# Performance work log

Hardware: AMD Instinct MI355X
Metric: run time of the kernel (lower is better)

The kernel has to match this reference:

```python
import jax, jax.numpy as jnp
import numpy as np

PARA_CH = 256
FEATURE_CH = 256
PI = 3.14159  # matches the literal in the torch source


def _linear_params(key, fan_in, fan_out):
    kw, kb = jax.random.split(key)
    bound = 1.0 / np.sqrt(fan_in)
    W = jax.random.uniform(kw, (fan_in, fan_out), minval=-bound, maxval=bound, dtype=jnp.float32)
    b = jax.random.uniform(kb, (fan_out,), minval=-bound, maxval=bound, dtype=jnp.float32)
    return W, b


def setup_inputs() -> dict:
    key = jax.random.key(0)
    ks = jax.random.split(key, 6)
    feature_map = jax.random.normal(ks[0], (4, FEATURE_CH, 128, 128), dtype=jnp.float32)
    para_code = jax.random.normal(ks[1], (4, PARA_CH), dtype=jnp.float32)
    W1, b1 = _linear_params(ks[2], PARA_CH, PARA_CH)
    Ws, bs = _linear_params(ks[3], PARA_CH, FEATURE_CH)
    Wr, br = _linear_params(ks[4], PARA_CH, FEATURE_CH)
    Wt, bt = _linear_params(ks[5], PARA_CH, 2 * FEATURE_CH)
    return {"feature_map": feature_map, "para_code": para_code,
            "W1": W1, "b1": b1, "Ws": Ws, "bs": bs,
            "Wr": Wr, "br": br, "Wt": Wt, "bt": bt}


def _coord_1d(n):
    # align_corners=True-style normalized coordinates, as in make_coordinate_grid_3d
    return 2.0 * (jnp.arange(n, dtype=jnp.float32) / (n - 1)) - 1.0


def _trilinear_sample_zeros(vol, gx, gy, gz):
    """F.grid_sample 5D equivalent: mode='bilinear' (trilinear), padding_mode='zeros',
    align_corners=False. vol: [B,D,H,W] (channel dim of size 1 squeezed out);
    gx,gy,gz: [B,Do,Ho,Wo] normalized coords. Returns [B,Do,Ho,Wo]."""
    B, D, H, W = vol.shape
    ix = ((gx + 1.0) * W - 1.0) * 0.5
    iy = ((gy + 1.0) * H - 1.0) * 0.5
    iz = ((gz + 1.0) * D - 1.0) * 0.5
    x0f, y0f, z0f = jnp.floor(ix), jnp.floor(iy), jnp.floor(iz)
    wx, wy, wz = ix - x0f, iy - y0f, iz - z0f
    x0 = x0f.astype(jnp.int32); x1 = x0 + 1
    y0 = y0f.astype(jnp.int32); y1 = y0 + 1
    z0 = z0f.astype(jnp.int32); z1 = z0 + 1
    vflat = vol.reshape(B, -1)

    def gather(zi, yi, xi):
        valid = (zi >= 0) & (zi < D) & (yi >= 0) & (yi < H) & (xi >= 0) & (xi < W)
        zc = jnp.clip(zi, 0, D - 1)
        yc = jnp.clip(yi, 0, H - 1)
        xc = jnp.clip(xi, 0, W - 1)
        flat = (zc * H + yc) * W + xc  # [B,Do,Ho,Wo]
        v = jnp.take_along_axis(vflat, flat.reshape(B, -1), axis=1).reshape(flat.shape)
        return jnp.where(valid, v, 0.0)

    out = (gather(z0, y0, x0) * (1 - wz) * (1 - wy) * (1 - wx)
           + gather(z0, y0, x1) * (1 - wz) * (1 - wy) * wx
           + gather(z0, y1, x0) * (1 - wz) * wy * (1 - wx)
           + gather(z0, y1, x1) * (1 - wz) * wy * wx
           + gather(z1, y0, x0) * wz * (1 - wy) * (1 - wx)
           + gather(z1, y0, x1) * wz * (1 - wy) * wx
           + gather(z1, y1, x0) * wz * wy * (1 - wx)
           + gather(z1, y1, x1) * wz * wy * wx)
    return out


def reference(feature_map, para_code, W1, b1, Ws, bs, Wr, br, Wt, bt):
    B, C, H, W = feature_map.shape  # C == feature_ch == depth of 3D grid
    p = jax.nn.relu(para_code @ W1 + b1)                      # [B, para_ch]
    scale = jax.nn.sigmoid(p @ Ws + bs) * 2.0                 # [B, C]
    angle = jnp.tanh(p @ Wr + br) * PI                        # [B, C]
    translation = jnp.tanh(p @ Wt + bt).reshape(B, C, 2)      # [B, C, 2]
    ca, sa = jnp.cos(angle), jnp.sin(angle)
    # rotation matrix [[cos, -sin], [sin, cos]] per (batch, channel)
    rot = jnp.stack([jnp.stack([ca, -sa], -1), jnp.stack([sa, ca], -1)], -2)  # [B,C,2,2]

    x = _coord_1d(W)  # [W]
    y = _coord_1d(H)  # [H]
    z = _coord_1d(C)  # [C] (depth == channel dim)
    grid_xy = jnp.stack(jnp.broadcast_arrays(x[None, None, :], y[None, :, None]), -1)  # [1,H,W,2] -> broadcast to [C,H,W,2]
    grid_xy = jnp.broadcast_to(grid_xy, (C, H, W, 2))

    # per-pixel affine transform: rot @ [x,y] * scale + trans
    trans_grid = jnp.einsum('bcij,chwj->bchwi', rot, grid_xy)
    trans_grid = trans_grid * scale[:, :, None, None, None] + translation[:, :, None, None, :]
    gx = trans_grid[..., 0]
    gy = trans_grid[..., 1]
    gz = jnp.broadcast_to(z[None, :, None, None], (B, C, H, W))

    return _trilinear_sample_zeros(feature_map, gx, gy, gz)  # [B,C,H,W]
```

## Files before the change

kernel.cpp:

```cpp
#include <hip/hip_runtime.h>
#include <math.h>

#define BATCH 4
#define CH    256
#define HH    128
#define WW    128
#define PC    256
#define PI_F  3.14159f
#define PLANE (HH * WW)
#define NP    4

__device__ __forceinline__ void barrier_lds() {
    asm volatile("s_waitcnt lgkmcnt(0)\n\ts_barrier" ::: "memory");
}

struct Stage { float4 a[4]; float4 b[4]; };

__device__ __forceinline__ Stage stage_load(const float* __restrict__ pl0,
                                            const float* __restrict__ pl1, int t) {
    Stage s;
#pragma unroll
    for (int j = 0; j < 4; ++j) {
        const int f = 4 * (t + 1024 * j);
        s.a[j] = *(const float4*)(pl0 + f);
        s.b[j] = *(const float4*)(pl1 + f);
    }
    return s;
}

__device__ __forceinline__ void stage_store(float* __restrict__ buf, const Stage& s,
                                            float wz0, float wz1, int t) {
#pragma unroll
    for (int j = 0; j < 4; ++j) {
        const int f = 4 * (t + 1024 * j);
        const int y = f >> 7, x = f & (WW - 1);
        float4 c;
        c.x = fmaf(wz0, s.a[j].x, wz1 * s.b[j].x);
        c.y = fmaf(wz0, s.a[j].y, wz1 * s.b[j].y);
        c.z = fmaf(wz0, s.a[j].z, wz1 * s.b[j].z);
        c.w = fmaf(wz0, s.a[j].w, wz1 * s.b[j].w);
        *(float4*)&buf[y * WW + (x ^ ((y & 3) << 3))] = c;
    }
}

__device__ __forceinline__ void gather_plane(const float* __restrict__ buf,
                                             const float4 P,
                                             float* __restrict__ outp,
                                             const float yf, const int xi) {
    const float cA = P.x, cB = P.y;
    const float Dx = fmaf(-P.y, yf, P.z);
    const float Dy = fmaf( P.x, yf, P.w);
#pragma unroll 2
    for (int k = 0; k < 16; ++k) {
        const float xf  = (float)(k * 8 + xi);
        const float ixf = fmaf(cA, xf, Dx);
        const float iyf = fmaf(cB, xf, Dy);
        const float x0f = floorf(ixf);
        const float y0f = floorf(iyf);
        const float fx  = ixf - x0f;
        const float fy  = iyf - y0f;
        const float mx0 = (x0f >= 0.0f  && x0f < 128.0f) ? (1.0f - fx) : 0.0f;
        const float mx1 = (x0f >= -1.0f && x0f < 127.0f) ? fx          : 0.0f;
        const float my0 = (y0f >= 0.0f  && y0f < 128.0f) ? (1.0f - fy) : 0.0f;
        const float my1 = (y0f >= -1.0f && y0f < 127.0f) ? fy          : 0.0f;

        const int x0i = (int)x0f, y0i = (int)y0f;
        const int xc0 = min(max(x0i,     0), WW - 1);
        const int xc1 = min(max(x0i + 1, 0), WW - 1);
        const int yc0 = min(max(y0i,     0), HH - 1);
        const int yc1 = min(max(y0i + 1, 0), HH - 1);

        const int r0 = yc0 * WW, r1 = yc1 * WW;
        const int s0 = (yc0 & 3) << 3, s1 = (yc1 & 3) << 3;
        const float v00 = buf[r0 + (xc0 ^ s0)];
        const float v01 = buf[r0 + (xc1 ^ s0)];
        const float v10 = buf[r1 + (xc0 ^ s1)];
        const float v11 = buf[r1 + (xc1 ^ s1)];

        outp[k * 8 + xi] = my0 * (mx0 * v00 + mx1 * v01)
                         + my1 * (mx0 * v10 + mx1 * v11);
    }
}

__global__ __launch_bounds__(1024, 4)
void adaat_fused_kernel(const float* __restrict__ fm,
                        const float* __restrict__ pc,
                        const float* __restrict__ W1, const float* __restrict__ b1,
                        const float* __restrict__ Ws, const float* __restrict__ bs,
                        const float* __restrict__ Wr, const float* __restrict__ br,
                        const float* __restrict__ Wt, const float* __restrict__ bt,
                        float* __restrict__ out) {
    __shared__ float  buf[2][PLANE];
    __shared__ float  p_sh[PC];
    __shared__ float  sh_head[16];
    __shared__ float4 sh_par[NP];

    const int t   = threadIdx.x;
    const int bc0 = blockIdx.x * NP;
    const int b   = bc0 >> 8;

    const float* base = fm + (size_t)b * (CH * PLANE);
    const float* pl0[NP]; const float* pl1[NP];
    float w0[NP], w1[NP];
#pragma unroll
    for (int i = 0; i < NP; ++i) {
        const int   c  = (bc0 + i) & (CH - 1);
        const float iz = (256.0f / 255.0f) * (float)c - 0.5f;
        const float zf = floorf(iz);
        const float fz = iz - zf;
        const int   z0 = (int)zf;
        w0[i]  = (z0 >= 0)     ? (1.0f - fz) : 0.0f;
        w1[i]  = (z0 + 1 < CH) ? fz          : 0.0f;
        pl0[i] = base + (size_t)max(z0, 0)          * PLANE;
        pl1[i] = base + (size_t)min(z0 + 1, CH - 1) * PLANE;
    }

    Stage s = stage_load(pl0[0], pl1[0], t);

    {
        float* red = &buf[1][0];
        const int jj = t & 255, kk = t >> 8;
        const float* pcb = pc + b * PC + kk * 64;
        const float* w   = W1 + (kk * 64) * PC + jj;
        float acc = 0.0f;
#pragma unroll 8
        for (int i = 0; i < 64; ++i)
            acc = fmaf(pcb[i], w[i * PC], acc);
        red[t] = acc;
        barrier_lds();
        if (t < 256)
            p_sh[t] = fmaxf(red[t] + red[256 + t] + red[512 + t] + red[768 + t] + b1[t], 0.0f);
        barrier_lds();
    }

    const int wv = t >> 6, l = t & 63;
    {
        const int q  = wv >> 2;
        const int h  = wv & 3;
        const int cq = (bc0 + q) & (CH - 1);
        const float* wp; int stride;
        if      (h == 0) { wp = Ws + cq;                stride = PC;     }
        else if (h == 1) { wp = Wr + cq;                stride = PC;     }
        else             { wp = Wt + 2 * cq + (h == 3); stride = 2 * PC; }
        float dot = 0.0f;
#pragma unroll
        for (int m = 0; m < 4; ++m) {
            const int k = l + 64 * m;
            dot = fmaf(p_sh[k], wp[(size_t)k * stride], dot);
        }
#pragma unroll
        for (int off = 32; off >= 1; off >>= 1)
            dot += __shfl_xor(dot, off, 64);
        if (l == 0) sh_head[wv] = dot;
    }
    barrier_lds();

    if (t < NP) {
        const int cq = (bc0 + t) & (CH - 1);
        const float s2  = 2.0f / (1.0f + expf(-(sh_head[4 * t] + bs[cq])));
        const float ang = tanhf(sh_head[4 * t + 1] + br[cq]) * PI_F;
        float sa, ca;
        sincosf(ang, &sa, &ca);
        const float A  = s2 * ca, B = s2 * sa;
        const float Tx = tanhf(sh_head[4 * t + 2] + bt[2 * cq]);
        const float Ty = tanhf(sh_head[4 * t + 3] + bt[2 * cq + 1]);
        sh_par[t] = make_float4(A * (128.0f / 127.0f),
                                B * (128.0f / 127.0f),
                                64.0f * (Tx - A + B) + 63.5f,
                                64.0f * (Ty - A - B) + 63.5f);
    }

    stage_store(&buf[0][0], s, w0[0], w1[0], t);
    barrier_lds();

    const int   xi = l & 7;
    const int   yj = wv * 8 + (l >> 3);
    const float yf = (float)yj;

#pragma unroll
    for (int i = 1; i < NP; ++i) {
        s = stage_load(pl0[i], pl1[i], t);
        gather_plane(&buf[(i - 1) & 1][0], sh_par[i - 1],
                     out + (size_t)(bc0 + i - 1) * PLANE + yj * WW, yf, xi);
        stage_store(&buf[i & 1][0], s, w0[i], w1[i], t);
        barrier_lds();
    }
    gather_plane(&buf[(NP - 1) & 1][0], sh_par[NP - 1],
                 out + (size_t)(bc0 + NP - 1) * PLANE + yj * WW, yf, xi);
}

extern "C" void kernel_launch(void* const* d_in, const int* in_sizes, int n_in,
                              void* d_out, int out_size, void* d_ws, size_t ws_size,
                              hipStream_t stream) {
    const float* feature_map = (const float*)d_in[0];
    const float* para_code   = (const float*)d_in[1];
    const float* W1 = (const float*)d_in[2];
    const float* b1 = (const float*)d_in[3];
    const float* Ws = (const float*)d_in[4];
    const float* bs = (const float*)d_in[5];
    const float* Wr = (const float*)d_in[6];
    const float* br = (const float*)d_in[7];
    const float* Wt = (const float*)d_in[8];
    const float* bt = (const float*)d_in[9];

    adaat_fused_kernel<<<BATCH * CH / NP, 1024, 0, stream>>>(
        feature_map, para_code, W1, b1, Ws, bs, Wr, br, Wt, bt, (float*)d_out);
}
```

Before: 157.7 us.

## Use zero-padded LDS plane to drop bounds masks in trilinear gather

```diff
diff --git a/kernel.cpp b/kernel.cpp
--- a/kernel.cpp
+++ b/kernel.cpp
@@ -10,6 +10,10 @@
 #define PLANE (HH * WW)
 #define NP    4
 
+#define PSTRIDE 134
+#define PROWS   131
+#define BUFSZ   (PROWS * PSTRIDE)
+
 __device__ __forceinline__ void barrier_lds() {
     asm volatile("s_waitcnt lgkmcnt(0)\n\ts_barrier" ::: "memory");
 }
@@ -28,18 +32,17 @@
     return s;
 }
 
-__device__ __forceinline__ void stage_store(float* __restrict__ buf, const Stage& s,
-                                            float wz0, float wz1, int t) {
+__device__ __forceinline__ void stage_store_pad(float* __restrict__ buf, const Stage& s,
+                                                float wz0, float wz1, int t) {
 #pragma unroll
     for (int j = 0; j < 4; ++j) {
         const int f = 4 * (t + 1024 * j);
         const int y = f >> 7, x = f & (WW - 1);
-        float4 c;
-        c.x = fmaf(wz0, s.a[j].x, wz1 * s.b[j].x);
-        c.y = fmaf(wz0, s.a[j].y, wz1 * s.b[j].y);
-        c.z = fmaf(wz0, s.a[j].z, wz1 * s.b[j].z);
-        c.w = fmaf(wz0, s.a[j].w, wz1 * s.b[j].w);
-        *(float4*)&buf[y * WW + (x ^ ((y & 3) << 3))] = c;
+        float* p = &buf[(y + 1) * PSTRIDE + (x + 1)];
+        p[0] = fmaf(wz0, s.a[j].x, wz1 * s.b[j].x);
+        p[1] = fmaf(wz0, s.a[j].y, wz1 * s.b[j].y);
+        p[2] = fmaf(wz0, s.a[j].z, wz1 * s.b[j].z);
+        p[3] = fmaf(wz0, s.a[j].w, wz1 * s.b[j].w);
     }
 }
 
@@ -47,38 +50,23 @@
                                              const float4 P,
                                              float* __restrict__ outp,
                                              const float yf, const int xi) {
-    const float cA = P.x, cB = P.y;
-    const float Dx = fmaf(-P.y, yf, P.z);
-    const float Dy = fmaf( P.x, yf, P.w);
-#pragma unroll 2
+    const float cA  = P.x, cB = P.y;
+    float ixp = fmaf(cA, (float)xi, fmaf(-cB, yf, P.z));
+    float iyp = fmaf(cB, (float)xi, fmaf( cA, yf, P.w));
+    const float dx8 = 8.0f * cA, dy8 = 8.0f * cB;
+#pragma unroll 4
     for (int k = 0; k < 16; ++k) {
-        const float xf  = (float)(k * 8 + xi);
-        const float ixf = fmaf(cA, xf, Dx);
-        const float iyf = fmaf(cB, xf, Dy);
-        const float x0f = floorf(ixf);
-        const float y0f = floorf(iyf);
-        const float fx  = ixf - x0f;
-        const float fy  = iyf - y0f;
-        const float mx0 = (x0f >= 0.0f  && x0f < 128.0f) ? (1.0f - fx) : 0.0f;
-        const float mx1 = (x0f >= -1.0f && x0f < 127.0f) ? fx          : 0.0f;
-        const float my0 = (y0f >= 0.0f  && y0f < 128.0f) ? (1.0f - fy) : 0.0f;
-        const float my1 = (y0f >= -1.0f && y0f < 127.0f) ? fy          : 0.0f;
-
-        const int x0i = (int)x0f, y0i = (int)y0f;
-        const int xc0 = min(max(x0i,     0), WW - 1);
-        const int xc1 = min(max(x0i + 1, 0), WW - 1);
-        const int yc0 = min(max(y0i,     0), HH - 1);
-        const int yc1 = min(max(y0i + 1, 0), HH - 1);
-
-        const int r0 = yc0 * WW, r1 = yc1 * WW;
-        const int s0 = (yc0 & 3) << 3, s1 = (yc1 & 3) << 3;
-        const float v00 = buf[r0 + (xc0 ^ s0)];
-        const float v01 = buf[r0 + (xc1 ^ s0)];
-        const float v10 = buf[r1 + (xc0 ^ s1)];
-        const float v11 = buf[r1 + (xc1 ^ s1)];
-
-        outp[k * 8 + xi] = my0 * (mx0 * v00 + mx1 * v01)
-                         + my1 * (mx0 * v10 + mx1 * v11);
+        const float xc  = fminf(fmaxf(ixp, 0.0f), 129.99f);
+        const float yc  = fminf(fmaxf(iyp, 0.0f), 129.99f);
+        const float x0f = floorf(xc), y0f = floorf(yc);
+        const float fx  = xc - x0f,   fy  = yc - y0f;
+        const int   a   = (int)y0f * PSTRIDE + (int)x0f;
+        const float v00 = buf[a],           v01 = buf[a + 1];
+        const float v10 = buf[a + PSTRIDE], v11 = buf[a + PSTRIDE + 1];
+        const float h0  = fmaf(fx, v01 - v00, v00);
+        const float h1  = fmaf(fx, v11 - v10, v10);
+        outp[k * 8 + xi] = fmaf(fy, h1 - h0, h0);
+        ixp += dx8; iyp += dy8;
     }
 }
 
@@ -90,7 +78,8 @@
                         const float* __restrict__ Wr, const float* __restrict__ br,
                         const float* __restrict__ Wt, const float* __restrict__ bt,
                         float* __restrict__ out) {
-    __shared__ float  buf[2][PLANE];
+    __shared__ float  lds[2 * BUFSZ];
+    __shared__ float  red[1024];
     __shared__ float  p_sh[PC];
     __shared__ float  sh_head[16];
     __shared__ float4 sh_par[NP];
@@ -117,8 +106,13 @@
 
     Stage s = stage_load(pl0[0], pl1[0], t);
 
+#pragma unroll
+    for (int i = 0; i < 35; ++i) {
+        const int idx = t + 1024 * i;
+        if (idx < 2 * BUFSZ) lds[idx] = 0.0f;
+    }
+
     {
-        float* red = &buf[1][0];
         const int jj = t & 255, kk = t >> 8;
         const float* pcb = pc + b * PC + kk * 64;
         const float* w   = W1 + (kk * 64) * PC + jj;
@@ -127,11 +121,13 @@
         for (int i = 0; i < 64; ++i)
             acc = fmaf(pcb[i], w[i * PC], acc);
         red[t] = acc;
-        barrier_lds();
-        if (t < 256)
-            p_sh[t] = fmaxf(red[t] + red[256 + t] + red[512 + t] + red[768 + t] + b1[t], 0.0f);
-        barrier_lds();
-    }
+    }
+    barrier_lds();
+    if (t < 256)
+        p_sh[t] = fmaxf(red[t] + red[256 + t] + red[512 + t] + red[768 + t] + b1[t], 0.0f);
+    barrier_lds();
+
+    stage_store_pad(&lds[0], s, w0[0], w1[0], t);
 
     const int wv = t >> 6, l = t & 63;
     {
@@ -166,11 +162,9 @@
         const float Ty = tanhf(sh_head[4 * t + 3] + bt[2 * cq + 1]);
         sh_par[t] = make_float4(A * (128.0f / 127.0f),
                                 B * (128.0f / 127.0f),
-                                64.0f * (Tx - A + B) + 63.5f,
-                                64.0f * (Ty - A - B) + 63.5f);
-    }
-
-    stage_store(&buf[0][0], s, w0[0], w1[0], t);
+                                64.0f * (Tx - A + B) + 64.5f,
+                                64.0f * (Ty - A - B) + 64.5f);
+    }
     barrier_lds();
 
     const int   xi = l & 7;
@@ -180,12 +174,12 @@
 #pragma unroll
     for (int i = 1; i < NP; ++i) {
         s = stage_load(pl0[i], pl1[i], t);
-        gather_plane(&buf[(i - 1) & 1][0], sh_par[i - 1],
+        gather_plane(&lds[((i - 1) & 1) * BUFSZ], sh_par[i - 1],
                      out + (size_t)(bc0 + i - 1) * PLANE + yj * WW, yf, xi);
-        stage_store(&buf[i & 1][0], s, w0[i], w1[i], t);
+        stage_store_pad(&lds[(i & 1) * BUFSZ], s, w0[i], w1[i], t);
         barrier_lds();
     }
-    gather_plane(&buf[(NP - 1) & 1][0], sh_par[NP - 1],
+    gather_plane(&lds[((NP - 1) & 1) * BUFSZ], sh_par[NP - 1],
                  out + (size_t)(bc0 + NP - 1) * PLANE + yj * WW, yf, xi);
 }
 
```

Result: faster. 150.9 us (-4.4%).
